# Kernel optimization log

Measured on AMD Instinct MI355X. Metric: run time of the kernel, lower is better.

## Reference

```python
import jax, jax.numpy as jnp
import numpy as np

N_NODES = 30000
N_EDGES = 480000
IN_CH = 64
CHANNELS = [64, 64, 64]
N_HEADS = 4
BN_EPS = 1e-5


def setup_inputs() -> dict:
    key = jax.random.key(0)
    ks = jax.random.split(key, 32)
    x = jax.random.normal(ks[0], (N_NODES, IN_CH), dtype=jnp.float32)
    # edges with no self loops (module removes then re-adds self loops)
    src = jax.random.randint(ks[1], (N_EDGES,), 0, N_NODES)
    off = jax.random.randint(ks[2], (N_EDGES,), 1, N_NODES)
    dst = (src + off) % N_NODES
    edge_index = jnp.stack([src, dst]).astype(jnp.int64)

    inp = {"x": x, "edge_index": edge_index}
    in_ch = IN_CH
    ki = 3
    for li, out_ch in enumerate(CHANNELS):
        # torch init: uniform_ for linear/u weights, N(0, 0.1) for c and bias
        inp[f"W{li}"] = jax.random.uniform(ks[ki], (out_ch * N_HEADS, in_ch), dtype=jnp.float32)
        inp[f"U{li}"] = jax.random.uniform(ks[ki + 1], (N_HEADS, in_ch), dtype=jnp.float32)
        inp[f"c{li}"] = 0.1 * jax.random.normal(ks[ki + 2], (N_HEADS,), dtype=jnp.float32)
        inp[f"b{li}"] = 0.1 * jax.random.normal(ks[ki + 3], (out_ch,), dtype=jnp.float32)
        if li < len(CHANNELS) - 1:  # BN only between layers
            inp[f"g{li}"] = jnp.ones((out_ch,), dtype=jnp.float32)
            inp[f"bt{li}"] = jnp.zeros((out_ch,), dtype=jnp.float32)
        ki += 4
        in_ch = out_ch
    return inp


def _feast_conv(x, src, dst, W, U, c, b, n_nodes):
    """FeatureSteeredConvolution with mean aggregation (trans-invariant attention)."""
    xi = x[dst]  # central nodes  [E, in]
    xj = x[src]  # neighbors      [E, in]
    logits = (xi - xj) @ U.T + c            # [E, M]
    attn = jax.nn.softmax(logits, axis=1)   # [E, M]
    e = src.shape[0]
    out_ch = W.shape[0] // N_HEADS
    xjw = (xj @ W.T).reshape(e, N_HEADS, out_ch)       # [E, M, out]
    msg = jnp.einsum('em,emo->eo', attn, xjw)           # [E, out]
    agg = jax.ops.segment_sum(msg, dst, num_segments=n_nodes)
    cnt = jax.ops.segment_sum(jnp.ones((e,), msg.dtype), dst, num_segments=n_nodes)
    return agg / cnt[:, None] + b  # self loops guarantee cnt >= 1


def _batch_norm(x, gamma, beta):
    # BatchNorm1d, training mode: biased batch statistics
    mu = x.mean(axis=0)
    var = x.var(axis=0)
    return (x - mu) * jax.lax.rsqrt(var + BN_EPS) * gamma + beta


def reference(x, edge_index, W0, U0, c0, b0, g0, bt0, W1, U1, c1, b1, g1, bt1, W2, U2, c2, b2):
    n = x.shape[0]
    loops = jnp.arange(n, dtype=edge_index.dtype)
    src = jnp.concatenate([edge_index[0], loops])
    dst = jnp.concatenate([edge_index[1], loops])
    h = _feast_conv(x, src, dst, W0, U0, c0, b0, n)
    h = _batch_norm(jax.nn.relu(h), g0, bt0)
    h = _feast_conv(h, src, dst, W1, U1, c1, b1, n)
    h = _batch_norm(jax.nn.relu(h), g1, bt1)
    return _feast_conv(h, src, dst, W2, U2, c2, b2, n)
```

## Files before the change

kernel.cpp:

```cpp
#include <hip/hip_runtime.h>

#define NN 30000
#define NE 480000
#define BN_EPS 1e-5f
#define EBLK 1875
#define FBLK 1875
#define PKBLK 469

typedef __attribute__((ext_vector_type(8))) short bf16x8;
typedef __attribute__((ext_vector_type(4))) float f32x4;

__device__ __forceinline__ unsigned short f2bf(float x) {
    unsigned int u = __float_as_uint(x);
    return (unsigned short)((u + 0x7fffu + ((u >> 16) & 1u)) >> 16);
}
__device__ __forceinline__ float bf2f(unsigned short h) {
    return __uint_as_float(((unsigned int)h) << 16);
}

__device__ __forceinline__ int detect64(const unsigned int* __restrict__ ei) {
    unsigned int v = ei[1] | ei[3] | ei[5] | ei[7] |
                     ei[9] | ei[11] | ei[13] | ei[15];
    return v == 0u;
}
__device__ __forceinline__ int load_idx(const void* ei, int is64, int pos) {
    if (is64) return (int)((const long long*)ei)[pos];
    return ((const int*)ei)[pos];
}

__global__ __launch_bounds__(256) void k_prep(const float* __restrict__ x,
                                              const float* __restrict__ W0,
                                              const float* __restrict__ W1,
                                              const float* __restrict__ W2,
                                              ushort* __restrict__ xbf,
                                              int4* __restrict__ zerobase,
                                              ushort* __restrict__ wb) {
    int t = blockIdx.x * 256 + threadIdx.x;
    if (t < 480000) {
        float4 v = reinterpret_cast<const float4*>(x)[t];
        ushort4 o;
        o.x = f2bf(v.x); o.y = f2bf(v.y); o.z = f2bf(v.z); o.w = f2bf(v.w);
        reinterpret_cast<ushort4*>(xbf)[t] = o;
    } else if (t < 480000 + 15064) {
        zerobase[t - 480000] = make_int4(0, 0, 0, 0);
    } else if (t < 480000 + 15064 + 49152) {
        int t2 = t - (480000 + 15064);
        int layer = t2 >> 14;
        int r = t2 & 16383;
        int ot = r >> 12;
        int kb = (r >> 9) & 7;
        int l = (r >> 3) & 63;
        int e = r & 7;
        int k = kb * 32 + (l >> 4) * 8 + e;
        int o = ot * 16 + (l & 15);
        int m = k >> 6;
        int kk = k & 63;
        const float* W = (layer == 0) ? W0 : (layer == 1) ? W1 : W2;
        wb[t2] = f2bf(W[(m * 64 + o) * 64 + kk]);
    }
}

__global__ __launch_bounds__(256) void k_hist(const void* __restrict__ ei,
                                              int* __restrict__ degi) {
    int e = blockIdx.x * 256 + threadIdx.x;
    int is64 = detect64((const unsigned int*)ei);
    int d = load_idx(ei, is64, NE + e);
    atomicAdd(&degi[d], 1);
}

__global__ __launch_bounds__(1024) void k_scan(const int* __restrict__ degi,
                                               int* __restrict__ rowptr) {
    __shared__ int sm[1024];
    const int PER = 30;
    int t = threadIdx.x;
    int base = t * PER;
    int loc[PER];
    int sum = 0;
#pragma unroll
    for (int i = 0; i < PER; ++i) {
        int idx = base + i;
        int d = (idx < NN) ? degi[idx] : 0;
        loc[i] = sum;
        sum += d;
    }
    sm[t] = sum;
    __syncthreads();
    for (int off = 1; off < 1024; off <<= 1) {
        int add = (t >= off) ? sm[t - off] : 0;
        __syncthreads();
        sm[t] += add;
        __syncthreads();
    }
    int tb = sm[t] - sum;
#pragma unroll
    for (int i = 0; i < PER; ++i) {
        int idx = base + i;
        if (idx < NN) rowptr[idx] = tb + loc[i];
    }
    if (t == 0) rowptr[NN] = NE;
}

template <int FOLD>
__device__ __forceinline__ void dev_pk(const float* __restrict__ h,
                                       const float* __restrict__ U,
                                       const float* __restrict__ stats,
                                       const float* __restrict__ g,
                                       float* __restrict__ pout, int vb) {
    __shared__ float usc_s[4][64];
    int t = threadIdx.x;
    {
        int m = t >> 6, k = t & 63;
        float sc = 1.0f;
        if (FOLD) {
            const float invN = 1.0f / (float)NN;
            float mu = stats[k] * invN;
            float var = stats[64 + k] * invN - mu * mu;
            sc = rsqrtf(var + BN_EPS) * g[k];
        }
        usc_s[m][k] = U[m * 64 + k] * sc;
    }
    __syncthreads();
    int idx = vb * 256 + t;
    if (idx < NN * 4) {
        int n = idx >> 2, m = idx & 3;
        const float4* hn = reinterpret_cast<const float4*>(h) + (size_t)n * 16;
        const float* um = usc_s[m];
        float a = 0.0f;
#pragma unroll
        for (int j = 0; j < 16; ++j) {
            float4 hv = hn[j];
            a += hv.x * um[4 * j + 0] + hv.y * um[4 * j + 1] +
                 hv.z * um[4 * j + 2] + hv.w * um[4 * j + 3];
        }
        pout[idx] = a;
    }
}

template <int FOLD>
__global__ __launch_bounds__(256) void k_pk(const float* __restrict__ h,
                                            const float* __restrict__ U,
                                            const float* __restrict__ stats,
                                            const float* __restrict__ g,
                                            const float* __restrict__ W,
                                            const float* __restrict__ bt,
                                            float* __restrict__ pout,
                                            float* __restrict__ cstv_out) {
    dev_pk<FOLD>(h, U, stats, g, pout, blockIdx.x);
    if (FOLD && blockIdx.x == 0) {
        int t = threadIdx.x;
        const float invN = 1.0f / (float)NN;
        float s = 0.0f;
        const float* wr = W + (size_t)t * 64;
#pragma unroll 8
        for (int k = 0; k < 64; ++k) {
            float mu = stats[k] * invN;
            float var = stats[64 + k] * invN - mu * mu;
            float sc = rsqrtf(var + BN_EPS) * g[k];
            float sh = bt[k] - mu * sc;
            s += sh * wr[k];
        }
        cstv_out[t] = s;
    }
}

__global__ __launch_bounds__(256) void k_scatter_pk0(const void* __restrict__ ei,
                                                     const int* __restrict__ rowptr,
                                                     int* __restrict__ cursor,
                                                     int* __restrict__ csr,
                                                     const float* __restrict__ x,
                                                     const float* __restrict__ U0,
                                                     float* __restrict__ p) {
    if (blockIdx.x < EBLK) {
        int is64 = detect64((const unsigned int*)ei);
        int e = blockIdx.x * 256 + threadIdx.x;
        int s = load_idx(ei, is64, e);
        int d = load_idx(ei, is64, NE + e);
        int pos = rowptr[d] + atomicAdd(&cursor[d], 1);
        csr[pos] = s;
    } else {
        dev_pk<0>(x, U0, nullptr, nullptr, p, blockIdx.x - EBLK);
    }
}

template <int FOLD, int STATS>
__global__ __launch_bounds__(1024, 8) void k_fused(const int* __restrict__ rowptr,
                                                   const int* __restrict__ csr,
                                                   const float* __restrict__ p,
                                                   const ushort* __restrict__ hbf_in,
                                                   const float* __restrict__ cvec,
                                                   const float* __restrict__ stats_in,
                                                   const float* __restrict__ g,
                                                   const float* __restrict__ cstvg,
                                                   const ushort* __restrict__ wb,
                                                   const float* __restrict__ bvec,
                                                   float* __restrict__ hout,
                                                   ushort* __restrict__ hbfout,
                                                   float* __restrict__ stats_out) {
    __shared__ float4 attn_s[16][64];
    __shared__ int src_s[16][64];
    __shared__ ushort zrow[16][264];
    __shared__ float4 zs_s[16];
    __shared__ float cstv_s[256];

    int t = threadIdx.x;
    int wid = t >> 6;
    int lane = t & 63;

    if (FOLD && t < 256) cstv_s[t] = cstvg[t];

    int n = blockIdx.x * 16 + wid;
    const float4* p4 = reinterpret_cast<const float4*>(p);

    float scl = 1.0f;
    if (FOLD) {
        const float invN = 1.0f / (float)NN;
        float mu = stats_in[lane] * invN;
        float var = stats_in[64 + lane] * invN - mu * mu;
        scl = rsqrtf(var + BN_EPS) * g[lane];
    }

    float4 cv = make_float4(cvec[0], cvec[1], cvec[2], cvec[3]);
    float smx = fmaxf(fmaxf(cv.x, cv.y), fmaxf(cv.z, cv.w));
    float se0 = __expf(cv.x - smx), se1 = __expf(cv.y - smx);
    float se2 = __expf(cv.z - smx), se3 = __expf(cv.w - smx);
    float sinv = 1.0f / (se0 + se1 + se2 + se3);
    float sl0 = se0 * sinv, sl1 = se1 * sinv, sl2 = se2 * sinv, sl3 = se3 * sinv;

    float4 pd = p4[n];
    float4 pdc = make_float4(pd.x + cv.x, pd.y + cv.y, pd.z + cv.z, pd.w + cv.w);
    float hs = bf2f(hbf_in[(unsigned)(n * 64 + lane)]);
    float acc0 = sl0 * hs, acc1 = sl1 * hs, acc2 = sl2 * hs, acc3 = sl3 * hs;
    float zt0 = sl0, zt1 = sl1, zt2 = sl2, zt3 = sl3;

    int start = rowptr[n];
    int end = rowptr[n + 1];
    for (int j = start; j < end; j += 64) {
        int chunk = end - j;
        if (chunk > 64) chunk = 64;
        if (lane < chunk) {
            int s = csr[j + lane];
            float4 q = p4[(unsigned)s];
            float l0 = pdc.x - q.x;
            float l1 = pdc.y - q.y;
            float l2 = pdc.z - q.z;
            float l3 = pdc.w - q.w;
            float mx = fmaxf(fmaxf(l0, l1), fmaxf(l2, l3));
            float e0 = __expf(l0 - mx);
            float e1 = __expf(l1 - mx);
            float e2 = __expf(l2 - mx);
            float e3 = __expf(l3 - mx);
            float inv = 1.0f / (e0 + e1 + e2 + e3);
            attn_s[wid][lane] = make_float4(e0 * inv, e1 * inv, e2 * inv, e3 * inv);
            src_s[wid][lane] = s;
        }
        int k = 0;
        for (; k + 4 <= chunk; k += 4) {
            float4 a0 = attn_s[wid][k];
            int s0 = src_s[wid][k];
            float4 a1 = attn_s[wid][k + 1];
            int s1 = src_s[wid][k + 1];
            float4 a2 = attn_s[wid][k + 2];
            int s2 = src_s[wid][k + 2];
            float4 a3 = attn_s[wid][k + 3];
            int s3 = src_s[wid][k + 3];
            float h0 = bf2f(hbf_in[(unsigned)(s0 * 64 + lane)]);
            float h1 = bf2f(hbf_in[(unsigned)(s1 * 64 + lane)]);
            float h2 = bf2f(hbf_in[(unsigned)(s2 * 64 + lane)]);
            float h3 = bf2f(hbf_in[(unsigned)(s3 * 64 + lane)]);
            acc0 += a0.x * h0 + a1.x * h1 + a2.x * h2 + a3.x * h3;
            acc1 += a0.y * h0 + a1.y * h1 + a2.y * h2 + a3.y * h3;
            acc2 += a0.z * h0 + a1.z * h1 + a2.z * h2 + a3.z * h3;
            acc3 += a0.w * h0 + a1.w * h1 + a2.w * h2 + a3.w * h3;
            zt0 += a0.x + a1.x + a2.x + a3.x;
            zt1 += a0.y + a1.y + a2.y + a3.y;
            zt2 += a0.z + a1.z + a2.z + a3.z;
            zt3 += a0.w + a1.w + a2.w + a3.w;
        }
        for (; k < chunk; ++k) {
            float4 a0 = attn_s[wid][k];
            int s0 = src_s[wid][k];
            float h0 = bf2f(hbf_in[(unsigned)(s0 * 64 + lane)]);
            acc0 += a0.x * h0;
            acc1 += a0.y * h0;
            acc2 += a0.z * h0;
            acc3 += a0.w * h0;
            zt0 += a0.x; zt1 += a0.y; zt2 += a0.z; zt3 += a0.w;
        }
    }

    float invD = 1.0f / (float)(end - start + 1);
    float s = invD * scl;
    {
        ushort* zr = &zrow[wid][0];
        zr[lane]        = f2bf(acc0 * s);
        zr[64 + lane]   = f2bf(acc1 * s);
        zr[128 + lane]  = f2bf(acc2 * s);
        zr[192 + lane]  = f2bf(acc3 * s);
        if (lane == 0)
            zs_s[wid] = make_float4(zt0 * invD, zt1 * invD, zt2 * invD, zt3 * invD);
    }
    __syncthreads();

    if (wid < 4) {
        int col = lane & 15;
        int grp = lane >> 4;
        int ot = wid;
        const ushort* zr = &zrow[col][grp * 8];
        const ushort* wbp = wb + ((size_t)(ot * 8) * 64 + lane) * 8;
        f32x4 acc = {0.0f, 0.0f, 0.0f, 0.0f};
#pragma unroll
        for (int kb = 0; kb < 8; ++kb) {
            bf16x8 a = *reinterpret_cast<const bf16x8*>(zr + kb * 32);
            bf16x8 b = *reinterpret_cast<const bf16x8*>(wbp + (size_t)kb * 512);
            acc = __builtin_amdgcn_mfma_f32_16x16x32_bf16(a, b, acc, 0, 0, 0);
        }

        int n0 = blockIdx.x * 16;
        int o = ot * 16 + col;
        float bval = bvec[o];
        float ls = 0.0f, lq = 0.0f;
#pragma unroll
        for (int i = 0; i < 4; ++i) {
            int nn = n0 + grp * 4 + i;
            float v = acc[i] + bval;
            if (FOLD) {
                float4 zv = zs_s[grp * 4 + i];
                v += zv.x * cstv_s[o] + zv.y * cstv_s[64 + o] +
                     zv.z * cstv_s[128 + o] + zv.w * cstv_s[192 + o];
            }
            if (STATS) {
                v = fmaxf(v, 0.0f);
                hout[(size_t)nn * 64 + o] = v;
                hbfout[(size_t)nn * 64 + o] = f2bf(v);
                ls += v;
                lq += v * v;
            } else {
                hout[(size_t)nn * 64 + o] = v;
            }
        }
        if (STATS) {
            ls += __shfl_xor(ls, 16, 64); ls += __shfl_xor(ls, 32, 64);
            lq += __shfl_xor(lq, 16, 64); lq += __shfl_xor(lq, 32, 64);
            if (lane < 16) {
                atomicAdd(&stats_out[o], ls);
                atomicAdd(&stats_out[64 + o], lq);
            }
        }
    }
}

extern "C" void kernel_launch(void* const* d_in, const int* in_sizes, int n_in,
                              void* d_out, int out_size, void* d_ws, size_t ws_size,
                              hipStream_t stream) {
    const float* x = (const float*)d_in[0];
    const void* ei = d_in[1];
    const float* W0 = (const float*)d_in[2];
    const float* U0 = (const float*)d_in[3];
    const float* c0 = (const float*)d_in[4];
    const float* b0 = (const float*)d_in[5];
    const float* g0 = (const float*)d_in[6];
    const float* bt0 = (const float*)d_in[7];
    const float* W1 = (const float*)d_in[8];
    const float* U1 = (const float*)d_in[9];
    const float* c1 = (const float*)d_in[10];
    const float* b1 = (const float*)d_in[11];
    const float* g1 = (const float*)d_in[12];
    const float* bt1 = (const float*)d_in[13];
    const float* W2 = (const float*)d_in[14];
    const float* U2 = (const float*)d_in[15];
    const float* c2 = (const float*)d_in[16];
    const float* b2 = (const float*)d_in[17];

    ushort* xbf = (ushort*)d_ws;
    ushort* hbfA = xbf + (size_t)NN * 64;
    ushort* hbfB = hbfA + (size_t)NN * 64;
    float* h = (float*)(hbfB + (size_t)NN * 64);
    float* p = h + (size_t)NN * 64;
    float* cstv = p + (size_t)NN * 4;
    int* degi = (int*)(cstv + 256);
    int* cursor = degi + NN;
    float* stats01 = (float*)(cursor + NN);
    int* rowptr = (int*)(stats01 + 256);
    int* csr = rowptr + NN + 4;
    ushort* wb = (ushort*)(csr + NE);
    float* stats0 = stats01;
    float* stats1 = stats01 + 128;

    const int prepBlocks = (480000 + 15064 + 49152 + 255) / 256;

    k_prep<<<prepBlocks, 256, 0, stream>>>(x, W0, W1, W2, xbf, (int4*)degi, wb);
    k_hist<<<EBLK, 256, 0, stream>>>(ei, degi);
    k_scan<<<1, 1024, 0, stream>>>(degi, rowptr);
    k_scatter_pk0<<<EBLK + PKBLK, 256, 0, stream>>>(ei, rowptr, cursor, csr,
                                                    x, U0, p);

    k_fused<0, 1><<<FBLK, 1024, 0, stream>>>(rowptr, csr, p, xbf, c0,
                                             nullptr, nullptr, nullptr,
                                             wb, b0, h, hbfA, stats0);
    k_pk<1><<<PKBLK, 256, 0, stream>>>(h, U1, stats0, g0, W1, bt0, p, cstv);
    k_fused<1, 1><<<FBLK, 1024, 0, stream>>>(rowptr, csr, p, hbfA, c1,
                                             stats0, g0, cstv,
                                             wb + 16384, b1, h, hbfB, stats1);
    k_pk<1><<<PKBLK, 256, 0, stream>>>(h, U2, stats1, g1, W2, bt1, p, cstv);
    k_fused<1, 0><<<FBLK, 1024, 0, stream>>>(rowptr, csr, p, hbfB, c2,
                                             stats1, g1, cstv,
                                             wb + 32768, b2, (float*)d_out,
                                             nullptr, nullptr);
}
```

Measured before the change: 311.4 us.

## Shrink fused blocks to 4 nodes with per-wave MFMA and sharded BN stats

The fused gather+GEMM kernel now uses 256-thread blocks handling 4 nodes, each wave doing its own 4 MFMA chains over all output tiles instead of block-wide sync and only 4 of 16 waves doing MFMA. This removes the __syncthreads and idle waves in the epilogue and raises block count. BN statistics atomics are spread over 16 shards to cut contention, with the reduction and scale computation moved into k_pk, which also writes the scale vector. Each wave now computes a 16-row MFMA for just one real row, wasting matrix throughput.

```diff
diff --git a/kernel.cpp b/kernel.cpp
--- a/kernel.cpp
+++ b/kernel.cpp
@@ -4,8 +4,9 @@
 #define NE 480000
 #define BN_EPS 1e-5f
 #define EBLK 1875
-#define FBLK 1875
+#define FBLK 7500
 #define PKBLK 469
+#define NSHARD 16
 
 typedef __attribute__((ext_vector_type(8))) short bf16x8;
 typedef __attribute__((ext_vector_type(4))) float f32x4;
@@ -41,10 +42,10 @@
         ushort4 o;
         o.x = f2bf(v.x); o.y = f2bf(v.y); o.z = f2bf(v.z); o.w = f2bf(v.w);
         reinterpret_cast<ushort4*>(xbf)[t] = o;
-    } else if (t < 480000 + 15064) {
+    } else if (t < 480000 + 16024) {
         zerobase[t - 480000] = make_int4(0, 0, 0, 0);
-    } else if (t < 480000 + 15064 + 49152) {
-        int t2 = t - (480000 + 15064);
+    } else if (t < 480000 + 16024 + 49152) {
+        int t2 = t - (480000 + 16024);
         int layer = t2 >> 14;
         int r = t2 & 16383;
         int ot = r >> 12;
@@ -100,24 +101,14 @@
     if (t == 0) rowptr[NN] = NE;
 }
 
-template <int FOLD>
-__device__ __forceinline__ void dev_pk(const float* __restrict__ h,
-                                       const float* __restrict__ U,
-                                       const float* __restrict__ stats,
-                                       const float* __restrict__ g,
-                                       float* __restrict__ pout, int vb) {
+__device__ __forceinline__ void dev_pk0(const float* __restrict__ h,
+                                        const float* __restrict__ U,
+                                        float* __restrict__ pout, int vb) {
     __shared__ float usc_s[4][64];
     int t = threadIdx.x;
     {
         int m = t >> 6, k = t & 63;
-        float sc = 1.0f;
-        if (FOLD) {
-            const float invN = 1.0f / (float)NN;
-            float mu = stats[k] * invN;
-            float var = stats[64 + k] * invN - mu * mu;
-            sc = rsqrtf(var + BN_EPS) * g[k];
-        }
-        usc_s[m][k] = U[m * 64 + k] * sc;
+        usc_s[m][k] = U[m * 64 + k];
     }
     __syncthreads();
     int idx = vb * 256 + t;
@@ -133,33 +124,6 @@
                  hv.z * um[4 * j + 2] + hv.w * um[4 * j + 3];
         }
         pout[idx] = a;
-    }
-}
-
-template <int FOLD>
-__global__ __launch_bounds__(256) void k_pk(const float* __restrict__ h,
-                                            const float* __restrict__ U,
-                                            const float* __restrict__ stats,
-                                            const float* __restrict__ g,
-                                            const float* __restrict__ W,
-                                            const float* __restrict__ bt,
-                                            float* __restrict__ pout,
-                                            float* __restrict__ cstv_out) {
-    dev_pk<FOLD>(h, U, stats, g, pout, blockIdx.x);
-    if (FOLD && blockIdx.x == 0) {
-        int t = threadIdx.x;
-        const float invN = 1.0f / (float)NN;
-        float s = 0.0f;
-        const float* wr = W + (size_t)t * 64;
-#pragma unroll 8
-        for (int k = 0; k < 64; ++k) {
-            float mu = stats[k] * invN;
-            float var = stats[64 + k] * invN - mu * mu;
-            float sc = rsqrtf(var + BN_EPS) * g[k];
-            float sh = bt[k] - mu * sc;
-            s += sh * wr[k];
-        }
-        cstv_out[t] = s;
     }
 }
 
@@ -178,46 +142,91 @@
         int pos = rowptr[d] + atomicAdd(&cursor[d], 1);
         csr[pos] = s;
     } else {
-        dev_pk<0>(x, U0, nullptr, nullptr, p, blockIdx.x - EBLK);
+        dev_pk0(x, U0, p, blockIdx.x - EBLK);
+    }
+}
+
+__global__ __launch_bounds__(256) void k_pk(const float* __restrict__ h,
+                                            const float* __restrict__ U,
+                                            const float* __restrict__ statsS,
+                                            const float* __restrict__ g,
+                                            const float* __restrict__ W,
+                                            const float* __restrict__ bt,
+                                            float* __restrict__ pout,
+                                            float* __restrict__ cstv_out,
+                                            float* __restrict__ scv_out) {
+    __shared__ float usc_s[4][64];
+    __shared__ float sc_l[64];
+    __shared__ float sh_l[64];
+    int t = threadIdx.x;
+    if (t < 64) {
+        float s1 = 0.0f, s2 = 0.0f;
+#pragma unroll
+        for (int sh = 0; sh < NSHARD; ++sh) {
+            s1 += statsS[sh * 128 + t];
+            s2 += statsS[sh * 128 + 64 + t];
+        }
+        const float invN = 1.0f / (float)NN;
+        float mu = s1 * invN;
+        float var = s2 * invN - mu * mu;
+        float sc = rsqrtf(var + BN_EPS) * g[t];
+        sc_l[t] = sc;
+        sh_l[t] = bt[t] - mu * sc;
+        if (blockIdx.x == 0) scv_out[t] = sc;
+    }
+    __syncthreads();
+    {
+        int m = t >> 6, k = t & 63;
+        usc_s[m][k] = U[m * 64 + k] * sc_l[k];
+    }
+    __syncthreads();
+    int idx = blockIdx.x * 256 + t;
+    if (idx < NN * 4) {
+        int n = idx >> 2, m = idx & 3;
+        const float4* hn = reinterpret_cast<const float4*>(h) + (size_t)n * 16;
+        const float* um = usc_s[m];
+        float a = 0.0f;
+#pragma unroll
+        for (int j = 0; j < 16; ++j) {
+            float4 hv = hn[j];
+            a += hv.x * um[4 * j + 0] + hv.y * um[4 * j + 1] +
+                 hv.z * um[4 * j + 2] + hv.w * um[4 * j + 3];
+        }
+        pout[idx] = a;
+    }
+    if (blockIdx.x == 0) {
+        float s = 0.0f;
+        const float* wr = W + (size_t)t * 64;
+#pragma unroll 8
+        for (int k = 0; k < 64; ++k) s += sh_l[k] * wr[k];
+        cstv_out[t] = s;
     }
 }
 
 template <int FOLD, int STATS>
-__global__ __launch_bounds__(1024, 8) void k_fused(const int* __restrict__ rowptr,
-                                                   const int* __restrict__ csr,
-                                                   const float* __restrict__ p,
-                                                   const ushort* __restrict__ hbf_in,
-                                                   const float* __restrict__ cvec,
-                                                   const float* __restrict__ stats_in,
-                                                   const float* __restrict__ g,
-                                                   const float* __restrict__ cstvg,
-                                                   const ushort* __restrict__ wb,
-                                                   const float* __restrict__ bvec,
-                                                   float* __restrict__ hout,
-                                                   ushort* __restrict__ hbfout,
-                                                   float* __restrict__ stats_out) {
-    __shared__ float4 attn_s[16][64];
-    __shared__ int src_s[16][64];
-    __shared__ ushort zrow[16][264];
-    __shared__ float4 zs_s[16];
-    __shared__ float cstv_s[256];
+__global__ __launch_bounds__(256, 4) void k_fused(const int* __restrict__ rowptr,
+                                                  const int* __restrict__ csr,
+                                                  const float* __restrict__ p,
+                                                  const ushort* __restrict__ hbf_in,
+                                                  const float* __restrict__ cvec,
+                                                  const float* __restrict__ scv,
+                                                  const float* __restrict__ cstv,
+                                                  const ushort* __restrict__ wb,
+                                                  const float* __restrict__ bvec,
+                                                  float* __restrict__ hout,
+                                                  ushort* __restrict__ hbfout,
+                                                  float* __restrict__ stats_out) {
+    __shared__ float4 attn_s[4][64];
+    __shared__ int src_s[4][64];
+    __shared__ ushort zrow[4][272];
 
     int t = threadIdx.x;
     int wid = t >> 6;
     int lane = t & 63;
-
-    if (FOLD && t < 256) cstv_s[t] = cstvg[t];
-
-    int n = blockIdx.x * 16 + wid;
+    int n = blockIdx.x * 4 + wid;
     const float4* p4 = reinterpret_cast<const float4*>(p);
 
-    float scl = 1.0f;
-    if (FOLD) {
-        const float invN = 1.0f / (float)NN;
-        float mu = stats_in[lane] * invN;
-        float var = stats_in[64 + lane] * invN - mu * mu;
-        scl = rsqrtf(var + BN_EPS) * g[lane];
-    }
+    float scl = FOLD ? scv[lane] : 1.0f;
 
     float4 cv = make_float4(cvec[0], cvec[1], cvec[2], cvec[3]);
     float smx = fmaxf(fmaxf(cv.x, cv.y), fmaxf(cv.z, cv.w));
@@ -290,62 +299,48 @@
 
     float invD = 1.0f / (float)(end - start + 1);
     float s = invD * scl;
-    {
-        ushort* zr = &zrow[wid][0];
-        zr[lane]        = f2bf(acc0 * s);
-        zr[64 + lane]   = f2bf(acc1 * s);
-        zr[128 + lane]  = f2bf(acc2 * s);
-        zr[192 + lane]  = f2bf(acc3 * s);
-        if (lane == 0)
-            zs_s[wid] = make_float4(zt0 * invD, zt1 * invD, zt2 * invD, zt3 * invD);
-    }
-    __syncthreads();
-
-    if (wid < 4) {
-        int col = lane & 15;
-        int grp = lane >> 4;
-        int ot = wid;
-        const ushort* zr = &zrow[col][grp * 8];
-        const ushort* wbp = wb + ((size_t)(ot * 8) * 64 + lane) * 8;
-        f32x4 acc = {0.0f, 0.0f, 0.0f, 0.0f};
-#pragma unroll
-        for (int kb = 0; kb < 8; ++kb) {
-            bf16x8 a = *reinterpret_cast<const bf16x8*>(zr + kb * 32);
-            bf16x8 b = *reinterpret_cast<const bf16x8*>(wbp + (size_t)kb * 512);
-            acc = __builtin_amdgcn_mfma_f32_16x16x32_bf16(a, b, acc, 0, 0, 0);
-        }
-
-        int n0 = blockIdx.x * 16;
-        int o = ot * 16 + col;
-        float bval = bvec[o];
-        float ls = 0.0f, lq = 0.0f;
-#pragma unroll
-        for (int i = 0; i < 4; ++i) {
-            int nn = n0 + grp * 4 + i;
-            float v = acc[i] + bval;
-            if (FOLD) {
-                float4 zv = zs_s[grp * 4 + i];
-                v += zv.x * cstv_s[o] + zv.y * cstv_s[64 + o] +
-                     zv.z * cstv_s[128 + o] + zv.w * cstv_s[192 + o];
-            }
-            if (STATS) {
-                v = fmaxf(v, 0.0f);
-                hout[(size_t)nn * 64 + o] = v;
-                hbfout[(size_t)nn * 64 + o] = f2bf(v);
-                ls += v;
-                lq += v * v;
-            } else {
-                hout[(size_t)nn * 64 + o] = v;
-            }
-        }
-        if (STATS) {
-            ls += __shfl_xor(ls, 16, 64); ls += __shfl_xor(ls, 32, 64);
-            lq += __shfl_xor(lq, 16, 64); lq += __shfl_xor(lq, 32, 64);
-            if (lane < 16) {
-                atomicAdd(&stats_out[o], ls);
-                atomicAdd(&stats_out[64 + o], lq);
-            }
-        }
+    ushort* zr = &zrow[wid][0];
+    zr[lane]       = f2bf(acc0 * s);
+    zr[64 + lane]  = f2bf(acc1 * s);
+    zr[128 + lane] = f2bf(acc2 * s);
+    zr[192 + lane] = f2bf(acc3 * s);
+
+    int grp = lane >> 4;
+    f32x4 ac0 = {0.0f, 0.0f, 0.0f, 0.0f};
+    f32x4 ac1 = {0.0f, 0.0f, 0.0f, 0.0f};
+    f32x4 ac2 = {0.0f, 0.0f, 0.0f, 0.0f};
+    f32x4 ac3 = {0.0f, 0.0f, 0.0f, 0.0f};
+#pragma unroll
+    for (int kb = 0; kb < 8; ++kb) {
+        bf16x8 a = *reinterpret_cast<const bf16x8*>(zr + kb * 32 + grp * 8);
+        const ushort* wk = wb + (size_t)(kb * 64 + lane) * 8;
+        bf16x8 b0 = *reinterpret_cast<const bf16x8*>(wk);
+        bf16x8 b1 = *reinterpret_cast<const bf16x8*>(wk + 4096);
+        bf16x8 b2 = *reinterpret_cast<const bf16x8*>(wk + 8192);
+        bf16x8 b3 = *reinterpret_cast<const bf16x8*>(wk + 12288);
+        ac0 = __builtin_amdgcn_mfma_f32_16x16x32_bf16(a, b0, ac0, 0, 0, 0);
+        ac1 = __builtin_amdgcn_mfma_f32_16x16x32_bf16(a, b1, ac1, 0, 0, 0);
+        ac2 = __builtin_amdgcn_mfma_f32_16x16x32_bf16(a, b2, ac2, 0, 0, 0);
+        ac3 = __builtin_amdgcn_mfma_f32_16x16x32_bf16(a, b3, ac3, 0, 0, 0);
+    }
+    float v = (grp == 0) ? ac0[0] : (grp == 1) ? ac1[0]
+            : (grp == 2) ? ac2[0] : ac3[0];
+
+    if (FOLD) {
+        v += (zt0 * cstv[lane] + zt1 * cstv[64 + lane] +
+              zt2 * cstv[128 + lane] + zt3 * cstv[192 + lane]) * invD;
+    }
+    v += bvec[lane];
+
+    if (STATS) {
+        v = fmaxf(v, 0.0f);
+        hout[(size_t)n * 64 + lane] = v;
+        hbfout[(size_t)n * 64 + lane] = f2bf(v);
+        float* so = stats_out + (blockIdx.x & (NSHARD - 1)) * 128;
+        atomicAdd(&so[lane], v);
+        atomicAdd(&so[64 + lane], v * v);
+    } else {
+        hout[(size_t)n * 64 + lane] = v;
     }
 }
 
@@ -377,16 +372,17 @@
     float* h = (float*)(hbfB + (size_t)NN * 64);
     float* p = h + (size_t)NN * 64;
     float* cstv = p + (size_t)NN * 4;
-    int* degi = (int*)(cstv + 256);
+    float* scv = cstv + 256;
+    int* degi = (int*)(scv + 64);
     int* cursor = degi + NN;
-    float* stats01 = (float*)(cursor + NN);
-    int* rowptr = (int*)(stats01 + 256);
+    float* statsA = (float*)(cursor + NN);
+    int* rowptr = (int*)(statsA + 4096);
     int* csr = rowptr + NN + 4;
     ushort* wb = (ushort*)(csr + NE);
-    float* stats0 = stats01;
-    float* stats1 = stats01 + 128;
-
-    const int prepBlocks = (480000 + 15064 + 49152 + 255) / 256;
+    float* stats0 = statsA;
+    float* stats1 = statsA + 2048;
+
+    const int prepBlocks = (480000 + 16024 + 49152 + 255) / 256;
 
     k_prep<<<prepBlocks, 256, 0, stream>>>(x, W0, W1, W2, xbf, (int4*)degi, wb);
     k_hist<<<EBLK, 256, 0, stream>>>(ei, degi);
@@ -394,16 +390,15 @@
     k_scatter_pk0<<<EBLK + PKBLK, 256, 0, stream>>>(ei, rowptr, cursor, csr,
                                                     x, U0, p);
 
-    k_fused<0, 1><<<FBLK, 1024, 0, stream>>>(rowptr, csr, p, xbf, c0,
-                                             nullptr, nullptr, nullptr,
-                                             wb, b0, h, hbfA, stats0);
-    k_pk<1><<<PKBLK, 256, 0, stream>>>(h, U1, stats0, g0, W1, bt0, p, cstv);
-    k_fused<1, 1><<<FBLK, 1024, 0, stream>>>(rowptr, csr, p, hbfA, c1,
-                                             stats0, g0, cstv,
-                                             wb + 16384, b1, h, hbfB, stats1);
-    k_pk<1><<<PKBLK, 256, 0, stream>>>(h, U2, stats1, g1, W2, bt1, p, cstv);
-    k_fused<1, 0><<<FBLK, 1024, 0, stream>>>(rowptr, csr, p, hbfB, c2,
-                                             stats1, g1, cstv,
-                                             wb + 32768, b2, (float*)d_out,
-                                             nullptr, nullptr);
-}
+    k_fused<0, 1><<<FBLK, 256, 0, stream>>>(rowptr, csr, p, xbf, c0,
+                                            nullptr, nullptr, wb, b0,
+                                            h, hbfA, stats0);
+    k_pk<<<PKBLK, 256, 0, stream>>>(h, U1, stats0, g0, W1, bt0, p, cstv, scv);
+    k_fused<1, 1><<<FBLK, 256, 0, stream>>>(rowptr, csr, p, hbfA, c1,
+                                            scv, cstv, wb + 16384, b1,
+                                            h, hbfB, stats1);
+    k_pk<<<PKBLK, 256, 0, stream>>>(h, U2, stats1, g1, W2, bt1, p, cstv, scv);
+    k_fused<1, 0><<<FBLK, 256, 0, stream>>>(rowptr, csr, p, hbfB, c2,
+                                            scv, cstv, wb + 32768, b2,
+                                            (float*)d_out, nullptr, nullptr);
+}
```

Result: slower. 367.7 us (+18.1%).
